# Optimization experiments

Measured on AMD Instinct MI355X. Metric: run time of the kernel, lower is better.

The kernel has to match this reference:

```python
import jax, jax.numpy as jnp
import numpy as np

B, T, N, F_IN, F_OUT = 2, 8, 8192, 128, 32

def setup_inputs() -> dict:
    key = jax.random.key(0)
    k1, k2, k3, k4 = jax.random.split(key, 4)
    inp = jax.random.normal(k1, (B, T, N, F_IN), dtype=jnp.float32)
    adj = jax.random.randint(k2, (N, N), 0, 2, dtype=jnp.int32)
    # xavier_uniform with gain=1.414 ~ std = gain*sqrt(2/(fan_in+fan_out)); gaussian approx
    w_std = 1.414 * np.sqrt(2.0 / (F_IN + F_OUT))
    a_std = 1.414 * np.sqrt(2.0 / (2 * F_OUT + N))
    W = jax.random.normal(k3, (F_IN, F_OUT), dtype=jnp.float32) * w_std
    a = jax.random.normal(k4, (2 * F_OUT, N), dtype=jnp.float32) * a_std
    return {"inp": inp, "adj": adj, "W": W, "a": a}

def reference(inp, adj, W, a):
    # h: [B,T,N,out]
    h = jnp.einsum('btni,io->btno', inp, W)
    out = W.shape[1]
    # mask[j,i] = 1 if j is a neighbor of i (original: torch.where(adj[:, i] > 0))
    mask = (adj > 0).astype(h.dtype)
    # neighbor sum per destination node i: [B,T,N,out]
    nbr = jnp.einsum('ji,btjo->btio', mask, h)
    a1 = a[:out].T   # [N, out], per-node first half of attention vector
    a2 = a[out:].T   # [N, out], per-node second half
    # scalar score per (b,t,i); broadcast across j in the original attention matrix.
    # no-neighbor case coincides since nbr is zero there.
    s = jnp.einsum('btno,no->btn', h, a1) + jnp.einsum('btno,no->btn', nbr, a2)
    # h_prime[b,t,i,:] = s[b,t,i] * sum_j h[b,t,j,:]  (attention row is constant)
    h_prime = s[..., None] * jnp.sum(h, axis=2, keepdims=True)
    return jax.nn.relu(h_prime)
```

## Files before the change

### kernel.cpp

```cpp
#include <hip/hip_runtime.h>

#define BT 16
#define NN 8192
#define FIN 128
#define FOUT 32
#define NB 512
#define SPLITK 4
#define KSPAN (NN / SPLITK)
#define BKK 64
#define PADK 72

typedef __attribute__((ext_vector_type(8))) short short8;
typedef __attribute__((ext_vector_type(4))) float float4v;

__device__ __forceinline__ float bf2f(unsigned short u) {
    unsigned v = ((unsigned)u) << 16;
    float f;
    __builtin_memcpy(&f, &v, 4);
    return f;
}
__device__ __forceinline__ unsigned short f2bf(float f) {
    unsigned u;
    __builtin_memcpy(&u, &f, 4);
    u += 0x7FFFu + ((u >> 16) & 1u);
    return (unsigned short)(u >> 16);
}

__device__ __forceinline__ void load_lds16(const unsigned short* g, unsigned short* l) {
    __builtin_amdgcn_global_load_lds((const __attribute__((address_space(1))) void*)g,
                                     (__attribute__((address_space(3))) void*)l, 16, 0, 0);
}

__global__ void sniff_dtype(const unsigned* __restrict__ Wraw, unsigned* __restrict__ flag,
                            float* __restrict__ sumh) {
    int lane = threadIdx.x;
    unsigned u = Wraw[lane];
    float f = bf2f((unsigned short)(u & 0xFFFFu));
    float af = fabsf(f);
    bool plaus = (af > 1e-5f) && (af < 1e3f);
    unsigned long long msk = __ballot(plaus);
    if (lane == 0) flag[0] = (__popcll(msk) >= 32) ? 1u : 0u;
#pragma unroll
    for (int r = 0; r < 8; ++r) sumh[lane + 64 * r] = 0.f;
}

__launch_bounds__(256)
__global__ void k1(const void* __restrict__ inp_raw, const void* __restrict__ W_raw,
                   unsigned short* __restrict__ Ht, float* __restrict__ sumh,
                   float4* __restrict__ s2v, const unsigned* __restrict__ flagp) {
    __shared__ __align__(16) unsigned short Wt[32 * 136];
    int bid = blockIdx.x;
    const int tid = threadIdx.x;

    if (bid < 128) {
        float4 z; z.x = z.y = z.z = z.w = 0.f;
        s2v[bid * 256 + tid] = z;
        return;
    }
    bid -= 128;
    const int bt = bid >> 6;
    const int j0 = (bid & 63) * 128;
    const bool isbf = (*flagp != 0u);

    if (isbf) {
        const unsigned short* Wb = (const unsigned short*)W_raw;
#pragma unroll
        for (int r = 0; r < 16; ++r) {
            int idx = tid + 256 * r, i = idx >> 5, o = idx & 31;
            Wt[o * 136 + i] = Wb[idx];
        }
    } else {
        const float* Wf = (const float*)W_raw;
#pragma unroll
        for (int r = 0; r < 16; ++r) {
            int idx = tid + 256 * r, i = idx >> 5, o = idx & 31;
            Wt[o * 136 + i] = f2bf(Wf[idx]);
        }
    }
    __syncthreads();

    const int lane = tid & 63, w = tid >> 6;
    const int m = lane & 15, q = lane >> 4;
    const int mt = (w & 1) * 16;
    const int nt = (w >> 1) * 64;

    float4v acc[4];
#pragma unroll
    for (int c = 0; c < 4; ++c) { float4v z = {0.f, 0.f, 0.f, 0.f}; acc[c] = z; }

#pragma unroll
    for (int kstep = 0; kstep < 4; ++kstep) {
        short8 af = *(const short8*)&Wt[(mt + m) * 136 + kstep * 32 + q * 8];
#pragma unroll
        for (int c = 0; c < 4; ++c) {
            int j = j0 + nt + c * 16 + m;
            short8 bfrag;
            if (isbf) {
                bfrag = *(const short8*)((const unsigned short*)inp_raw +
                        ((size_t)bt * NN + j) * FIN + kstep * 32 + q * 8);
            } else {
                const float* fp = (const float*)inp_raw + ((size_t)bt * NN + j) * FIN + kstep * 32 + q * 8;
                float4 f0 = *(const float4*)fp;
                float4 f1 = *(const float4*)(fp + 4);
                union { unsigned short u[8]; short8 v; } t;
                t.u[0] = f2bf(f0.x); t.u[1] = f2bf(f0.y); t.u[2] = f2bf(f0.z); t.u[3] = f2bf(f0.w);
                t.u[4] = f2bf(f1.x); t.u[5] = f2bf(f1.y); t.u[6] = f2bf(f1.z); t.u[7] = f2bf(f1.w);
                bfrag = t.v;
            }
            acc[c] = __builtin_amdgcn_mfma_f32_16x16x32_bf16(af, bfrag, acc[c], 0, 0, 0);
        }
    }

#pragma unroll
    for (int c = 0; c < 4; ++c) {
#pragma unroll
        for (int e = 0; e < 4; ++e) {
            int o = mt + q * 4 + e;
            int j = j0 + nt + c * 16 + m;
            Ht[(size_t)(bt * FOUT + o) * NN + j] = f2bf(acc[c][e]);
        }
    }
#pragma unroll
    for (int e = 0; e < 4; ++e) {
        float s = acc[0][e] + acc[1][e] + acc[2][e] + acc[3][e];
        s += __shfl_xor(s, 1); s += __shfl_xor(s, 2);
        s += __shfl_xor(s, 4); s += __shfl_xor(s, 8);
        if (m == 0) atomicAdd(&sumh[bt * FOUT + mt + q * 4 + e], s);
    }
}

__launch_bounds__(512, 4)
__global__ void k2_fused(const int* __restrict__ adj, const unsigned short* __restrict__ Ht,
                         const void* __restrict__ a_raw, float* __restrict__ s2,
                         const unsigned* __restrict__ flagp) {
    __shared__ __align__(16) unsigned short As[64 * PADK];
    __shared__ __align__(16) unsigned short Bs[512 * 64];
    const int tid = threadIdx.x;
    const int lane = tid & 63;
    const int w = tid >> 6;
    const int m = lane & 15, q = lane >> 4;
    const int wn = w * 64;

    const int bid = blockIdx.x;
    const int xcd = bid & 7;
    const int z = xcd >> 1;
    const int ib = (bid >> 3) | ((xcd & 1) << 6);
    const int i0 = ib * 64;
    const int zbase = z * KSPAN;

    const int* gcol = adj + (zbase + w * 8) * NN + i0 + lane;

    float4v acc[4][4];
#pragma unroll
    for (int r = 0; r < 4; ++r)
#pragma unroll
        for (int c = 0; c < 4; ++c) { float4v zz = {0.f, 0.f, 0.f, 0.f}; acc[r][c] = zz; }

    for (int ks0 = 0; ks0 < KSPAN; ks0 += BKK) {
        const int k0 = zbase + ks0;
        __syncthreads();
        int av[8];
#pragma unroll
        for (int kk = 0; kk < 8; ++kk)
            av[kk] = gcol[(ks0 + kk) * NN];
#pragma unroll
        for (int c = 0; c < 8; ++c) {
            int u = (w * 8 + c) * 64 + lane;
            int n = u >> 3;
            int kbs = (u & 7) ^ (n & 7);
            load_lds16(Ht + n * NN + kbs * 8 + k0, &Bs[(w * 8 + c) * 512]);
        }
        {
            unsigned d0 = (av[0] > 0 ? 0x3F80u : 0u) | (av[1] > 0 ? 0x3F800000u : 0u);
            unsigned d1 = (av[2] > 0 ? 0x3F80u : 0u) | (av[3] > 0 ? 0x3F800000u : 0u);
            unsigned d2 = (av[4] > 0 ? 0x3F80u : 0u) | (av[5] > 0 ? 0x3F800000u : 0u);
            unsigned d3 = (av[6] > 0 ? 0x3F80u : 0u) | (av[7] > 0 ? 0x3F800000u : 0u);
            int4 t;
            t.x = (int)d0; t.y = (int)d1; t.z = (int)d2; t.w = (int)d3;
            *(int4*)&As[lane * PADK + w * 8] = t;
        }
        __syncthreads();
#pragma unroll
        for (int ks = 0; ks < 2; ++ks) {
            short8 af[4];
#pragma unroll
            for (int r = 0; r < 4; ++r)
                af[r] = *(const short8*)&As[(r * 16 + m) * PADK + ks * 32 + q * 8];
#pragma unroll
            for (int c = 0; c < 4; ++c) {
                int row = wn + c * 16 + m;
                int kbs = (ks * 4 + q) ^ (m & 7);
                short8 bfr = *(const short8*)&Bs[row * 64 + kbs * 8];
#pragma unroll
                for (int r = 0; r < 4; ++r)
                    acc[r][c] = __builtin_amdgcn_mfma_f32_16x16x32_bf16(af[r], bfr, acc[r][c], 0, 0, 0);
            }
        }
    }

    const bool isbf = (*flagp != 0u);
    const int btA = wn >> 5;
#pragma unroll
    for (int r = 0; r < 4; ++r) {
#pragma unroll
        for (int e = 0; e < 4; ++e) {
            int gi = i0 + r * 16 + q * 4 + e;
            float a2m, a2m16;
            if (isbf) {
                const unsigned short* ab = (const unsigned short*)a_raw;
                a2m   = bf2f(ab[(size_t)(FOUT + m) * NN + gi]);
                a2m16 = bf2f(ab[(size_t)(FOUT + 16 + m) * NN + gi]);
            } else {
                const float* afp = (const float*)a_raw;
                a2m   = afp[(size_t)(FOUT + m) * NN + gi];
                a2m16 = afp[(size_t)(FOUT + 16 + m) * NN + gi];
            }
            float sA = acc[r][0][e] * a2m + acc[r][1][e] * a2m16;
            float sB = acc[r][2][e] * a2m + acc[r][3][e] * a2m16;
            sA += __shfl_xor(sA, 1); sA += __shfl_xor(sA, 2);
            sA += __shfl_xor(sA, 4); sA += __shfl_xor(sA, 8);
            sB += __shfl_xor(sB, 1); sB += __shfl_xor(sB, 2);
            sB += __shfl_xor(sB, 4); sB += __shfl_xor(sB, 8);
            if (m == 0) {
                atomicAdd(&s2[(size_t)btA * NN + gi], sA);
                atomicAdd(&s2[(size_t)(btA + 1) * NN + gi], sB);
            }
        }
    }
}

__launch_bounds__(256)
__global__ void k3_out(const unsigned short* __restrict__ Ht, const float* __restrict__ s2,
                       const float* __restrict__ sumh, const void* __restrict__ a_raw,
                       void* __restrict__ out_raw, const unsigned* __restrict__ flagp) {
    const int i = blockIdx.x * 256 + threadIdx.x;
    const int bt = blockIdx.y;
    const bool isbf = (*flagp != 0u);

    float s = s2[(size_t)bt * NN + i];
    if (isbf) {
        const unsigned short* ab = (const unsigned short*)a_raw;
#pragma unroll
        for (int o = 0; o < 32; ++o) {
            float h = bf2f(Ht[(size_t)(bt * FOUT + o) * NN + i]);
            s += h * bf2f(ab[(size_t)o * NN + i]);
        }
    } else {
        const float* afp = (const float*)a_raw;
#pragma unroll
        for (int o = 0; o < 32; ++o) {
            float h = bf2f(Ht[(size_t)(bt * FOUT + o) * NN + i]);
            s += h * afp[(size_t)o * NN + i];
        }
    }

    float ov[32];
#pragma unroll
    for (int o = 0; o < 32; ++o) ov[o] = fmaxf(s * sumh[bt * FOUT + o], 0.f);

    size_t ob = ((size_t)bt * NN + i) * FOUT;
    if (isbf) {
        unsigned short* o16 = (unsigned short*)out_raw + ob;
#pragma unroll
        for (int c = 0; c < 8; ++c) {
            ushort4 p;
            p.x = f2bf(ov[c * 4 + 0]); p.y = f2bf(ov[c * 4 + 1]);
            p.z = f2bf(ov[c * 4 + 2]); p.w = f2bf(ov[c * 4 + 3]);
            *(ushort4*)(o16 + c * 4) = p;
        }
    } else {
        float* of = (float*)out_raw + ob;
#pragma unroll
        for (int c = 0; c < 8; ++c) {
            float4 v;
            v.x = ov[c * 4 + 0]; v.y = ov[c * 4 + 1]; v.z = ov[c * 4 + 2]; v.w = ov[c * 4 + 3];
            *(float4*)(of + c * 4) = v;
        }
    }
}

extern "C" void kernel_launch(void* const* d_in, const int* in_sizes, int n_in,
                              void* d_out, int out_size, void* d_ws, size_t ws_size,
                              hipStream_t stream) {
    const void* inp = d_in[0];
    const int* adj = (const int*)d_in[1];
    const void* W = d_in[2];
    const void* a = d_in[3];

    char* ws = (char*)d_ws;
    unsigned short* Ht = (unsigned short*)ws;
    unsigned* flag = (unsigned*)(ws + 8388608);
    float* s2 = (float*)(ws + 8388608 + 4096);
    float* sumh = (float*)(ws + 8388608 + 4096 + 524288);

    sniff_dtype<<<1, 64, 0, stream>>>((const unsigned*)W, flag, sumh);
    k1<<<1152, 256, 0, stream>>>(inp, W, Ht, sumh, (float4*)s2, flag);
    k2_fused<<<512, 512, 0, stream>>>(adj, Ht, a, s2, flag);
    k3_out<<<dim3(NN / 256, BT), 256, 0, stream>>>(Ht, s2, sumh, a, d_out, flag);
}
```

Baseline: 488.0 us.

## Double-buffer adjacency and H tiles in k2 with BK=32 software pipeline

Restructures the k2 main loop into a two-stage software pipeline. LDS tiles for the adjacency mask and Ht are double-buffered, and the K tile shrinks from 64 to 32. Global loads for the next tiles are issued before the MFMAs on the current tile, and there is one barrier per step instead of two. The aim is to hide global/LDS load latency behind the matrix cores. The cost is twice as many loop iterations, and wrapped indices mean some redundant loads are issued on the final iterations.

```diff
diff --git a/kernel.cpp b/kernel.cpp
--- a/kernel.cpp
+++ b/kernel.cpp
@@ -7,8 +7,9 @@
 #define NB 512
 #define SPLITK 4
 #define KSPAN (NN / SPLITK)
-#define BKK 64
-#define PADK 72
+#define BKK 32
+#define NT 64
+#define PADA 40
 
 typedef __attribute__((ext_vector_type(8))) short short8;
 typedef __attribute__((ext_vector_type(4))) float float4v;
@@ -133,8 +134,8 @@
 __global__ void k2_fused(const int* __restrict__ adj, const unsigned short* __restrict__ Ht,
                          const void* __restrict__ a_raw, float* __restrict__ s2,
                          const unsigned* __restrict__ flagp) {
-    __shared__ __align__(16) unsigned short As[64 * PADK];
-    __shared__ __align__(16) unsigned short Bs[512 * 64];
+    __shared__ __align__(16) unsigned short As[2][64 * PADA];
+    __shared__ __align__(16) unsigned short Bs[2][512 * 32];
     const int tid = threadIdx.x;
     const int lane = tid & 63;
     const int w = tid >> 6;
@@ -148,7 +149,18 @@
     const int i0 = ib * 64;
     const int zbase = z * KSPAN;
 
-    const int* gcol = adj + (zbase + w * 8) * NN + i0 + lane;
+    int boff[4];
+#pragma unroll
+    for (int c = 0; c < 4; ++c) {
+        int u = (w * 4 + c) * 64 + lane;
+        int n = u >> 2;
+        int kbs = (u & 3) ^ (n & 3);
+        boff[c] = n * NN + kbs * 8;
+    }
+
+    const int* gcol = adj + (zbase + w * 4) * NN + i0 + lane;
+    unsigned short* asw0 = &As[0][lane * PADA + w * 4];
+    unsigned short* asw1 = &As[1][lane * PADA + w * 4];
 
     float4v acc[4][4];
 #pragma unroll
@@ -156,45 +168,80 @@
 #pragma unroll
         for (int c = 0; c < 4; ++c) { float4v zz = {0.f, 0.f, 0.f, 0.f}; acc[r][c] = zz; }
 
-    for (int ks0 = 0; ks0 < KSPAN; ks0 += BKK) {
-        const int k0 = zbase + ks0;
-        __syncthreads();
-        int av[8];
-#pragma unroll
-        for (int kk = 0; kk < 8; ++kk)
-            av[kk] = gcol[(ks0 + kk) * NN];
-#pragma unroll
-        for (int c = 0; c < 8; ++c) {
-            int u = (w * 8 + c) * 64 + lane;
-            int n = u >> 3;
-            int kbs = (u & 7) ^ (n & 7);
-            load_lds16(Ht + n * NN + kbs * 8 + k0, &Bs[(w * 8 + c) * 512]);
-        }
+    int avA[4], avB[4];
+
+#pragma unroll
+    for (int kk = 0; kk < 4; ++kk) avB[kk] = gcol[kk * NN];
+#pragma unroll
+    for (int c = 0; c < 4; ++c)
+        load_lds16(Ht + boff[c] + zbase, &Bs[0][(w * 4 + c) * 512]);
+#pragma unroll
+    for (int kk = 0; kk < 4; ++kk) avA[kk] = gcol[(BKK + kk) * NN];
+    {
+        unsigned d0 = (avB[0] > 0 ? 0x3F80u : 0u) | (avB[1] > 0 ? 0x3F800000u : 0u);
+        unsigned d1 = (avB[2] > 0 ? 0x3F80u : 0u) | (avB[3] > 0 ? 0x3F800000u : 0u);
+        int2 t; t.x = (int)d0; t.y = (int)d1;
+        *(int2*)asw0 = t;
+    }
+    __syncthreads();
+
+#pragma unroll 1
+    for (int t2 = 0; t2 < NT; t2 += 2) {
         {
-            unsigned d0 = (av[0] > 0 ? 0x3F80u : 0u) | (av[1] > 0 ? 0x3F800000u : 0u);
-            unsigned d1 = (av[2] > 0 ? 0x3F80u : 0u) | (av[3] > 0 ? 0x3F800000u : 0u);
-            unsigned d2 = (av[4] > 0 ? 0x3F80u : 0u) | (av[5] > 0 ? 0x3F800000u : 0u);
-            unsigned d3 = (av[6] > 0 ? 0x3F80u : 0u) | (av[7] > 0 ? 0x3F800000u : 0u);
-            int4 t;
-            t.x = (int)d0; t.y = (int)d1; t.z = (int)d2; t.w = (int)d3;
-            *(int4*)&As[lane * PADK + w * 8] = t;
-        }
-        __syncthreads();
-#pragma unroll
-        for (int ks = 0; ks < 2; ++ks) {
+            const int tg = (t2 + 1) & (NT - 1);
+            const int tn = (t2 + 2) & (NT - 1);
+#pragma unroll
+            for (int kk = 0; kk < 4; ++kk)
+                avB[kk] = gcol[(tn * BKK + kk) * NN];
+#pragma unroll
+            for (int c = 0; c < 4; ++c)
+                load_lds16(Ht + boff[c] + zbase + tg * BKK, &Bs[1][(w * 4 + c) * 512]);
             short8 af[4];
 #pragma unroll
             for (int r = 0; r < 4; ++r)
-                af[r] = *(const short8*)&As[(r * 16 + m) * PADK + ks * 32 + q * 8];
+                af[r] = *(const short8*)&As[0][(r * 16 + m) * PADA + q * 8];
 #pragma unroll
             for (int c = 0; c < 4; ++c) {
                 int row = wn + c * 16 + m;
-                int kbs = (ks * 4 + q) ^ (m & 7);
-                short8 bfr = *(const short8*)&Bs[row * 64 + kbs * 8];
+                int kbs = q ^ (m & 3);
+                short8 bfr = *(const short8*)&Bs[0][row * 32 + kbs * 8];
 #pragma unroll
                 for (int r = 0; r < 4; ++r)
                     acc[r][c] = __builtin_amdgcn_mfma_f32_16x16x32_bf16(af[r], bfr, acc[r][c], 0, 0, 0);
             }
+            unsigned d0 = (avA[0] > 0 ? 0x3F80u : 0u) | (avA[1] > 0 ? 0x3F800000u : 0u);
+            unsigned d1 = (avA[2] > 0 ? 0x3F80u : 0u) | (avA[3] > 0 ? 0x3F800000u : 0u);
+            int2 t; t.x = (int)d0; t.y = (int)d1;
+            *(int2*)asw1 = t;
+            __syncthreads();
+        }
+        {
+            const int tg = (t2 + 2) & (NT - 1);
+            const int tn = (t2 + 3) & (NT - 1);
+#pragma unroll
+            for (int kk = 0; kk < 4; ++kk)
+                avA[kk] = gcol[(tn * BKK + kk) * NN];
+#pragma unroll
+            for (int c = 0; c < 4; ++c)
+                load_lds16(Ht + boff[c] + zbase + tg * BKK, &Bs[0][(w * 4 + c) * 512]);
+            short8 af[4];
+#pragma unroll
+            for (int r = 0; r < 4; ++r)
+                af[r] = *(const short8*)&As[1][(r * 16 + m) * PADA + q * 8];
+#pragma unroll
+            for (int c = 0; c < 4; ++c) {
+                int row = wn + c * 16 + m;
+                int kbs = q ^ (m & 3);
+                short8 bfr = *(const short8*)&Bs[1][row * 32 + kbs * 8];
+#pragma unroll
+                for (int r = 0; r < 4; ++r)
+                    acc[r][c] = __builtin_amdgcn_mfma_f32_16x16x32_bf16(af[r], bfr, acc[r][c], 0, 0, 0);
+            }
+            unsigned d0 = (avB[0] > 0 ? 0x3F80u : 0u) | (avB[1] > 0 ? 0x3F800000u : 0u);
+            unsigned d1 = (avB[2] > 0 ? 0x3F80u : 0u) | (avB[3] > 0 ? 0x3F800000u : 0u);
+            int2 t; t.x = (int)d0; t.y = (int)d1;
+            *(int2*)asw0 = t;
+            __syncthreads();
         }
     }
 
```

Result: slower. 535.6 us (+9.8%).

## Prepack adjacency mask into LDS bitmask and shrink K tile

Applied to the files above, without the earlier changes.

At block start, each block now reads its full adjacency slice once and packs it into an LDS bitmask with wave ballots. The main loop then builds the bf16 mask tile from LDS bits instead of strided global int loads. The K tile is halved to 32 so the LDS budget fits the new bitmask buffer. This trades more iterations and barriers, plus a serial prologue, for removing adjacency global loads from the inner loop.

```diff
diff --git a/kernel.cpp b/kernel.cpp
--- a/kernel.cpp
+++ b/kernel.cpp
@@ -7,8 +7,9 @@
 #define NB 512
 #define SPLITK 4
 #define KSPAN (NN / SPLITK)
-#define BKK 64
-#define PADK 72
+#define BKK 32
+#define NT 64
+#define PADA 40
 
 typedef __attribute__((ext_vector_type(8))) short short8;
 typedef __attribute__((ext_vector_type(4))) float float4v;
@@ -133,8 +134,9 @@
 __global__ void k2_fused(const int* __restrict__ adj, const unsigned short* __restrict__ Ht,
                          const void* __restrict__ a_raw, float* __restrict__ s2,
                          const unsigned* __restrict__ flagp) {
-    __shared__ __align__(16) unsigned short As[64 * PADK];
-    __shared__ __align__(16) unsigned short Bs[512 * 64];
+    __shared__ int Pl[KSPAN * 2];
+    __shared__ __align__(16) unsigned short As[64 * PADA];
+    __shared__ __align__(16) unsigned short Bs[512 * 32];
     const int tid = threadIdx.x;
     const int lane = tid & 63;
     const int w = tid >> 6;
@@ -148,7 +150,34 @@
     const int i0 = ib * 64;
     const int zbase = z * KSPAN;
 
-    const int* gcol = adj + (zbase + w * 8) * NN + i0 + lane;
+    {
+        const int* arow = adj + (size_t)zbase * NN + i0 + lane;
+        for (int r0 = 0; r0 < 256; r0 += 16) {
+            int v[16];
+#pragma unroll
+            for (int j = 0; j < 16; ++j)
+                v[j] = arow[(size_t)(w * 256 + r0 + j) * NN];
+#pragma unroll
+            for (int j = 0; j < 16; ++j) {
+                unsigned long long b = __ballot(v[j] > 0);
+                if (lane == 0) {
+                    int k = w * 256 + r0 + j;
+                    int2 t;
+                    t.x = (int)(unsigned)(b & 0xFFFFFFFFull);
+                    t.y = (int)(unsigned)(b >> 32);
+                    *(int2*)&Pl[k * 2] = t;
+                }
+            }
+        }
+    }
+
+    int boff[4];
+#pragma unroll
+    for (int c = 0; c < 4; ++c) {
+        int u = (w * 4 + c) * 64 + lane;
+        int kbs = (u & 3) ^ ((u >> 3) & 3);
+        boff[c] = (u >> 2) * NN + kbs * 8;
+    }
 
     float4v acc[4][4];
 #pragma unroll
@@ -156,46 +185,39 @@
 #pragma unroll
         for (int c = 0; c < 4; ++c) { float4v zz = {0.f, 0.f, 0.f, 0.f}; acc[r][c] = zz; }
 
-    for (int ks0 = 0; ks0 < KSPAN; ks0 += BKK) {
-        const int k0 = zbase + ks0;
+    __syncthreads();
+
+    for (int t = 0; t < NT; ++t) {
+#pragma unroll
+        for (int c = 0; c < 4; ++c)
+            load_lds16(Ht + boff[c] + zbase + t * BKK, &Bs[(w * 4 + c) * 512]);
+        {
+            const int kb = t * BKK + w * 4;
+            const int h = lane >> 5, sh = lane & 31;
+            unsigned w0 = ((unsigned)Pl[(kb + 0) * 2 + h] >> sh) & 1u;
+            unsigned w1 = ((unsigned)Pl[(kb + 1) * 2 + h] >> sh) & 1u;
+            unsigned w2 = ((unsigned)Pl[(kb + 2) * 2 + h] >> sh) & 1u;
+            unsigned w3 = ((unsigned)Pl[(kb + 3) * 2 + h] >> sh) & 1u;
+            int2 tt;
+            tt.x = (int)((w0 ? 0x3F80u : 0u) | (w1 ? 0x3F800000u : 0u));
+            tt.y = (int)((w2 ? 0x3F80u : 0u) | (w3 ? 0x3F800000u : 0u));
+            *(int2*)&As[lane * PADA + w * 4] = tt;
+        }
         __syncthreads();
-        int av[8];
-#pragma unroll
-        for (int kk = 0; kk < 8; ++kk)
-            av[kk] = gcol[(ks0 + kk) * NN];
-#pragma unroll
-        for (int c = 0; c < 8; ++c) {
-            int u = (w * 8 + c) * 64 + lane;
-            int n = u >> 3;
-            int kbs = (u & 7) ^ (n & 7);
-            load_lds16(Ht + n * NN + kbs * 8 + k0, &Bs[(w * 8 + c) * 512]);
-        }
-        {
-            unsigned d0 = (av[0] > 0 ? 0x3F80u : 0u) | (av[1] > 0 ? 0x3F800000u : 0u);
-            unsigned d1 = (av[2] > 0 ? 0x3F80u : 0u) | (av[3] > 0 ? 0x3F800000u : 0u);
-            unsigned d2 = (av[4] > 0 ? 0x3F80u : 0u) | (av[5] > 0 ? 0x3F800000u : 0u);
-            unsigned d3 = (av[6] > 0 ? 0x3F80u : 0u) | (av[7] > 0 ? 0x3F800000u : 0u);
-            int4 t;
-            t.x = (int)d0; t.y = (int)d1; t.z = (int)d2; t.w = (int)d3;
-            *(int4*)&As[lane * PADK + w * 8] = t;
+        short8 af[4];
+#pragma unroll
+        for (int r = 0; r < 4; ++r)
+            af[r] = *(const short8*)&As[(r * 16 + m) * PADA + q * 8];
+#pragma unroll
+        for (int c = 0; c < 4; ++c) {
+            int row = wn + c * 16 + m;
+            int kbs = q ^ ((m >> 1) & 3);
+            short8 bfr = *(const short8*)&Bs[row * 32 + kbs * 8];
+#pragma unroll
+            for (int r = 0; r < 4; ++r)
+                acc[r][c] = __builtin_amdgcn_mfma_f32_16x16x32_bf16(af[r], bfr, acc[r][c], 0, 0, 0);
         }
         __syncthreads();
-#pragma unroll
-        for (int ks = 0; ks < 2; ++ks) {
-            short8 af[4];
-#pragma unroll
-            for (int r = 0; r < 4; ++r)
-                af[r] = *(const short8*)&As[(r * 16 + m) * PADK + ks * 32 + q * 8];
-#pragma unroll
-            for (int c = 0; c < 4; ++c) {
-                int row = wn + c * 16 + m;
-                int kbs = (ks * 4 + q) ^ (m & 7);
-                short8 bfr = *(const short8*)&Bs[row * 64 + kbs * 8];
-#pragma unroll
-                for (int r = 0; r < 4; ++r)
-                    acc[r][c] = __builtin_amdgcn_mfma_f32_16x16x32_bf16(af[r], bfr, acc[r][c], 0, 0, 0);
-            }
-        }
     }
 
     const bool isbf = (*flagp != 0u);
```

Result: slower. 539.6 us (+10.6%).

## Prepack adjacency into LDS bitmasks and stream Ht directly from global

Applied to the files above, without the earlier changes.

The k2_fused kernel now reads its whole adjacency K-span up front with nontemporal loads and packs it into 32-bit bitmasks in a small LDS array. The per-iteration LDS staging of Ht and the two barriers per K-step are gone. Each lane instead loads its B fragments straight from global memory and expands bitmask bytes into bf16 A fragments in registers. This cuts LDS footprint and synchronization, which could raise occupancy, but it relies on cache hits for Ht reuse across waves and adds ALU work for the bit expansion.

```diff
diff --git a/kernel.cpp b/kernel.cpp
--- a/kernel.cpp
+++ b/kernel.cpp
@@ -7,8 +7,6 @@
 #define NB 512
 #define SPLITK 4
 #define KSPAN (NN / SPLITK)
-#define BKK 64
-#define PADK 72
 
 typedef __attribute__((ext_vector_type(8))) short short8;
 typedef __attribute__((ext_vector_type(4))) float float4v;
@@ -24,11 +22,6 @@
     __builtin_memcpy(&u, &f, 4);
     u += 0x7FFFu + ((u >> 16) & 1u);
     return (unsigned short)(u >> 16);
-}
-
-__device__ __forceinline__ void load_lds16(const unsigned short* g, unsigned short* l) {
-    __builtin_amdgcn_global_load_lds((const __attribute__((address_space(1))) void*)g,
-                                     (__attribute__((address_space(3))) void*)l, 16, 0, 0);
 }
 
 __global__ void sniff_dtype(const unsigned* __restrict__ Wraw, unsigned* __restrict__ flag,
@@ -133,8 +126,7 @@
 __global__ void k2_fused(const int* __restrict__ adj, const unsigned short* __restrict__ Ht,
                          const void* __restrict__ a_raw, float* __restrict__ s2,
                          const unsigned* __restrict__ flagp) {
-    __shared__ __align__(16) unsigned short As[64 * PADK];
-    __shared__ __align__(16) unsigned short Bs[512 * 64];
+    __shared__ int Pl[64 * 65];
     const int tid = threadIdx.x;
     const int lane = tid & 63;
     const int w = tid >> 6;
@@ -148,7 +140,24 @@
     const int i0 = ib * 64;
     const int zbase = z * KSPAN;
 
-    const int* gcol = adj + (zbase + w * 8) * NN + i0 + lane;
+    {
+        const int* arow = adj + (size_t)(zbase + w * 256) * NN + i0 + lane;
+#pragma unroll
+        for (int u = 0; u < 8; ++u) {
+            unsigned wv = 0;
+            const int* gp = arow + (size_t)(u * 32) * NN;
+#pragma unroll
+            for (int j = 0; j < 32; ++j)
+                wv |= (__builtin_nontemporal_load(gp + (size_t)j * NN) > 0 ? 1u : 0u) << j;
+            Pl[lane * 65 + w * 8 + u] = (int)wv;
+        }
+    }
+    __syncthreads();
+
+    const unsigned short* bp[4];
+#pragma unroll
+    for (int c = 0; c < 4; ++c)
+        bp[c] = Ht + (size_t)(wn + c * 16 + m) * NN + zbase + q * 8;
 
     float4v acc[4][4];
 #pragma unroll
@@ -156,46 +165,29 @@
 #pragma unroll
         for (int c = 0; c < 4; ++c) { float4v zz = {0.f, 0.f, 0.f, 0.f}; acc[r][c] = zz; }
 
-    for (int ks0 = 0; ks0 < KSPAN; ks0 += BKK) {
-        const int k0 = zbase + ks0;
-        __syncthreads();
-        int av[8];
-#pragma unroll
-        for (int kk = 0; kk < 8; ++kk)
-            av[kk] = gcol[(ks0 + kk) * NN];
-#pragma unroll
-        for (int c = 0; c < 8; ++c) {
-            int u = (w * 8 + c) * 64 + lane;
-            int n = u >> 3;
-            int kbs = (u & 7) ^ (n & 7);
-            load_lds16(Ht + n * NN + kbs * 8 + k0, &Bs[(w * 8 + c) * 512]);
-        }
-        {
-            unsigned d0 = (av[0] > 0 ? 0x3F80u : 0u) | (av[1] > 0 ? 0x3F800000u : 0u);
-            unsigned d1 = (av[2] > 0 ? 0x3F80u : 0u) | (av[3] > 0 ? 0x3F800000u : 0u);
-            unsigned d2 = (av[4] > 0 ? 0x3F80u : 0u) | (av[5] > 0 ? 0x3F800000u : 0u);
-            unsigned d3 = (av[6] > 0 ? 0x3F80u : 0u) | (av[7] > 0 ? 0x3F800000u : 0u);
-            int4 t;
-            t.x = (int)d0; t.y = (int)d1; t.z = (int)d2; t.w = (int)d3;
-            *(int4*)&As[lane * PADK + w * 8] = t;
-        }
-        __syncthreads();
-#pragma unroll
-        for (int ks = 0; ks < 2; ++ks) {
-            short8 af[4];
+#pragma unroll 4
+    for (int t = 0; t < 64; ++t) {
+        short8 bfr[4];
+#pragma unroll
+        for (int c = 0; c < 4; ++c)
+            bfr[c] = *(const short8*)(bp[c] + t * 32);
+        short8 af[4];
+#pragma unroll
+        for (int r = 0; r < 4; ++r) {
+            unsigned word = (unsigned)Pl[(r * 16 + m) * 65 + t];
+            unsigned byt = (word >> (q * 8)) & 0xFFu;
+            union { unsigned d[4]; short8 v; } tt;
+            tt.d[0] = (byt & 1u   ? 0x3F80u : 0u) | (byt & 2u   ? 0x3F800000u : 0u);
+            tt.d[1] = (byt & 4u   ? 0x3F80u : 0u) | (byt & 8u   ? 0x3F800000u : 0u);
+            tt.d[2] = (byt & 16u  ? 0x3F80u : 0u) | (byt & 32u  ? 0x3F800000u : 0u);
+            tt.d[3] = (byt & 64u  ? 0x3F80u : 0u) | (byt & 128u ? 0x3F800000u : 0u);
+            af[r] = tt.v;
+        }
+#pragma unroll
+        for (int c = 0; c < 4; ++c)
 #pragma unroll
             for (int r = 0; r < 4; ++r)
-                af[r] = *(const short8*)&As[(r * 16 + m) * PADK + ks * 32 + q * 8];
-#pragma unroll
-            for (int c = 0; c < 4; ++c) {
-                int row = wn + c * 16 + m;
-                int kbs = (ks * 4 + q) ^ (m & 7);
-                short8 bfr = *(const short8*)&Bs[row * 64 + kbs * 8];
-#pragma unroll
-                for (int r = 0; r < 4; ++r)
-                    acc[r][c] = __builtin_amdgcn_mfma_f32_16x16x32_bf16(af[r], bfr, acc[r][c], 0, 0, 0);
-            }
-        }
+                acc[r][c] = __builtin_amdgcn_mfma_f32_16x16x32_bf16(af[r], bfr[c], acc[r][c], 0, 0, 0);
     }
 
     const bool isbf = (*flagp != 0u);
```

After: 557.0 us. 1.14x slower.
